# Kernel optimization log

Measured on AMD Instinct MI355X. Metric: run time of the kernel, lower is better.

The kernel has to match this reference:

```python
import jax, jax.numpy as jnp
import numpy as np

LAT, LONG = 16, 12
C_IN, C_MID = 128, 128
GROUPS = C_IN // 8          # conv groups and GroupNorm groups = 16
E = 200_000                 # number of projection entries (edges)
N = 4096                    # out_size (number of target messages)
PAD = LONG // 2
EPS = 1e-5


def setup_inputs() -> dict:
    key = jax.random.key(0)
    ks = jax.random.split(key, 8)
    x = jax.random.normal(ks[0], (E, C_IN), dtype=jnp.float32)
    proj_index = jax.random.randint(ks[1], (4, E), 0, N * LAT * LONG, dtype=jnp.int64 if jax.config.jax_enable_x64 else jnp.int32)
    proj_delta = jax.random.uniform(ks[2], (4, E), dtype=jnp.float32)
    proj_src_index = jax.random.randint(ks[3], (E,), 0, E, dtype=jnp.int64 if jax.config.jax_enable_x64 else jnp.int32)
    # grouped circular Conv1d: weight [out, in/groups, k] = [128, 2048/16, 12]
    fan_in = (C_IN * LAT // GROUPS) * LONG
    bound = 1.0 / np.sqrt(fan_in)
    conv_w = jax.random.uniform(ks[4], (C_MID, C_IN * LAT // GROUPS, LONG), dtype=jnp.float32, minval=-bound, maxval=bound)
    conv_b = jax.random.uniform(ks[5], (C_MID,), dtype=jnp.float32, minval=-bound, maxval=bound)
    gn_w = jnp.ones((C_MID,), dtype=jnp.float32)
    gn_b = jnp.zeros((C_MID,), dtype=jnp.float32)
    return {"x": x, "out_size": N, "proj_index": proj_index, "proj_delta": proj_delta,
            "proj_src_index": proj_src_index, "conv_w": conv_w, "conv_b": conv_b,
            "gn_w": gn_w, "gn_b": gn_b}


def reference(x, out_size, proj_index, proj_delta, proj_src_index, conv_w, conv_b, gn_w, gn_b):
    # ---- ProjectLatLongSphere: 4 weighted scatter-adds onto the sphere grid ----
    splat = x[proj_src_index]                              # [E, C]
    x_proj = jnp.zeros((out_size * LAT * LONG, C_IN), dtype=x.dtype)
    for i in range(4):                                      # fixed small unroll
        x_proj = x_proj.at[proj_index[i]].add(splat * proj_delta[i][:, None])
    # [N, lat*long, C] -> [N, C, lat*long] -> [N, C*lat, long]
    x_grid = x_proj.reshape(out_size, LAT * LONG, C_IN).transpose(0, 2, 1)
    x_grid = x_grid.reshape(out_size, C_IN * LAT, LONG)

    # ---- grouped circular Conv1d ----
    xp = jnp.concatenate([x_grid[..., -PAD:], x_grid, x_grid[..., :PAD]], axis=-1)  # [N, C*lat, long+2*pad]
    y = jax.lax.conv_general_dilated(
        xp, conv_w, window_strides=(1,), padding='VALID',
        dimension_numbers=('NCH', 'OIH', 'NCH'), feature_group_count=GROUPS)        # [N, C_MID, long+1]
    y = jax.nn.silu(y + conv_b[None, :, None])

    # ---- AvgPool1d(kernel=long) over first `long` positions ----
    y = jnp.mean(y[:, :, :LONG], axis=-1)                   # [N, C_MID]

    # ---- GroupNorm(num_groups=GROUPS) on [N, C_MID] ----
    g = y.reshape(out_size, GROUPS, C_MID // GROUPS)
    mu = jnp.mean(g, axis=-1, keepdims=True)
    var = jnp.var(g, axis=-1, keepdims=True)
    g = (g - mu) * jax.lax.rsqrt(var + EPS)
    return g.reshape(out_size, C_MID) * gn_w + gn_b
```

## Files before the change

kernel.cpp:

```cpp
#include <hip/hip_runtime.h>
#include <hip/hip_fp16.h>
#include <cstdint>

#define LATN 16
#define LONGN 12
#define PP 192
#define CIN 128
#define CMID 128
#define EPSV 1e-5f
#define SPLIT 4
#define CHB 32
#define TST 36
#define UMAXA 4

typedef float v2f __attribute__((ext_vector_type(2)));
typedef float f32x4 __attribute__((ext_vector_type(4)));
typedef _Float16 half8 __attribute__((ext_vector_type(8)));


__global__ void count2_kernel(const int* __restrict__ pidx, int* __restrict__ counts, int E) {
    int e = blockIdx.x * 256 + threadIdx.x;
    if (e >= E) return;
#pragma unroll
    for (int i = 0; i < 4; i++) {
        int v = pidx[i * E + e];
        atomicAdd(&counts[v], 1);
    }
}

__global__ void scan1_kernel(const int* __restrict__ cnt, int* __restrict__ startp,
                             int* __restrict__ bsum) {
    __shared__ int sd[1024];
    int t = threadIdx.x, b = blockIdx.x;
    int v = cnt[b * 1024 + t];
    sd[t] = v;
    __syncthreads();
    for (int off = 1; off < 1024; off <<= 1) {
        int x = (t >= off) ? sd[t - off] : 0;
        __syncthreads();
        sd[t] += x;
        __syncthreads();
    }
    startp[b * 1024 + t] = sd[t] - v;
    if (t == 1023) bsum[b] = sd[t];
}

__global__ void scan2_kernel(int* __restrict__ bsum, int* __restrict__ grand, int nb) {
    __shared__ int sd[1024];
    int t = threadIdx.x;
    int v = (t < nb) ? bsum[t] : 0;
    sd[t] = v;
    __syncthreads();
    for (int off = 1; off < 1024; off <<= 1) {
        int x = (t >= off) ? sd[t - off] : 0;
        __syncthreads();
        sd[t] += x;
        __syncthreads();
    }
    if (t < nb) bsum[t] = sd[t] - v;
    if (t == 1023) *grand = sd[1023];
}

__global__ void addback_kernel(int* __restrict__ startp, const int* __restrict__ bsum,
                               int* __restrict__ cur) {
    int v = blockIdx.x * 1024 + threadIdx.x;
    int s = startp[v] + bsum[blockIdx.x];
    startp[v] = s;
    cur[v] = s;
}

__global__ void record_kernel(const int* __restrict__ pidx, const int* __restrict__ src_idx,
                              const float* __restrict__ delta, int* __restrict__ cur,
                              uint2* __restrict__ rec, int E) {
    int e = blockIdx.x * 256 + threadIdx.x;
    if (e >= E) return;
    int src = src_idx[e];
#pragma unroll
    for (int i = 0; i < 4; i++) {
        int v = pidx[i * E + e];
        int p = v - (v / PP) * PP;
        int pos = atomicAdd(&cur[v], 1);
        rec[pos] = make_uint2((uint32_t)src | ((uint32_t)p << 18),
                              __float_as_uint(delta[i * E + e]));
    }
}

__global__ void wt2_kernel(const float* __restrict__ w, uint32_t* __restrict__ wt2) {
    int id = blockIdx.x * 256 + threadIdx.x;
    if (id >= CIN * 6 * CMID) return;
    int o = id & 127;
    int kp = (id >> 7) % 6;
    int i = id / (128 * 6);
    float a = w[(o * 128 + i) * 12 + 2 * kp];
    float b = w[(o * 128 + i) * 12 + 2 * kp + 1];
    __half2 h = __floats2half2_rn(a, b);
    wt2[id] = *reinterpret_cast<uint32_t*>(&h);
}


__global__ void wA_kernel(const float* __restrict__ w, _Float16* __restrict__ wA) {
    int id = blockIdx.x * 256 + threadIdx.x;
    if (id >= 16 * 6 * 48 * 64) return;
    int lane = id & 63;
    int rest = id >> 6;
    int s = rest % 48;
    int mt = (rest / 48) % 6;
    int g = rest / (48 * 6);
    int m = mt * 16 + (lane & 15);
    int o = m / 12;
    int t = m - o * 12;
    int og = g * 8 + o;
    _Float16 vals[8];
#pragma unroll
    for (int j = 0; j < 8; j++) {
        int kh = s * 32 + (lane >> 4) * 8 + j;
        int c = kh / PP;
        int p = kh - c * PP;
        int lat = p / LONGN;
        int ll = p - lat * LONGN;
        int k = (ll - t + 18) % 12;
        vals[j] = (_Float16)w[((og)*128 + c * 16 + lat) * 12 + k];
    }
    *(uint4*)(wA + (size_t)id * 8) = *(const uint4*)vals;
}


__global__ __launch_bounds__(256, 5) void scatter_kernel(
    const float* __restrict__ x, const uint2* __restrict__ rec,
    const int* __restrict__ start2, _Float16* __restrict__ grid) {
    __shared__ __align__(16) float tile[PP * TST];
    __shared__ int s2c[PP + 1];

    const int bid = blockIdx.x;
    const int n = bid >> 2;
    const int b = bid & 3;
    const int tid = threadIdx.x;

    {
        float4 zz = {0.f, 0.f, 0.f, 0.f};
        float4* t4 = (float4*)tile;
        for (int idx = tid; idx < PP * TST / 4; idx += 256) t4[idx] = zz;
        for (int idx = tid; idx < PP + 1; idx += 256) s2c[idx] = start2[n * PP + idx];
    }
    __syncthreads();

    {
        const int il = tid & 7;
        const int slot = tid >> 3;
        const int cbase = b * CHB + il * 4;
        const int e1 = s2c[slot * 6 + 6];
        for (int e = s2c[slot * 6]; e < e1; e += UMAXA) {
            uint2 rv[UMAXA];
            float4 xv[UMAXA];
#pragma unroll
            for (int u = 0; u < UMAXA; u++) {
                if (e + u < e1) rv[u] = rec[e + u];
            }
#pragma unroll
            for (int u = 0; u < UMAXA; u++) {
                if (e + u < e1) {
                    int src = (int)(rv[u].x & 0x3FFFFu);
                    xv[u] = *(const float4*)(x + (size_t)src * CIN + cbase);
                }
            }
#pragma unroll
            for (int u = 0; u < UMAXA; u++) {
                if (e + u < e1) {
                    float dl = __uint_as_float(rv[u].y);
                    int p = (int)(rv[u].x >> 18);
                    float* tp = tile + p * TST + (((il + (p & 7)) & 7) << 2);
                    float4 t = *(const float4*)tp;
                    t.x += xv[u].x * dl;
                    t.y += xv[u].y * dl;
                    t.z += xv[u].z * dl;
                    t.w += xv[u].w * dl;
                    *(float4*)tp = t;
                }
            }
        }
    }
    __syncthreads();

    {
        const int c = tid & 31;
        const int pc = tid >> 5;
        const int gch = b * CHB + c;
        _Float16* gdst = grid + ((size_t)n * CIN + gch) * PP;
        const int il = c >> 2;
        const int cm = c & 3;
#pragma unroll
        for (int j16 = 0; j16 < 3; j16++) {
            int pbase = pc * 24 + j16 * 8;
            _Float16 hh[8];
#pragma unroll
            for (int i = 0; i < 8; i++) {
                int p = pbase + i;
                hh[i] = (_Float16)tile[p * TST + ((((il + (p & 7)) & 7) << 2) + cm)];
            }
            *(uint4*)(gdst + pbase) = *(const uint4*)hh;
        }
    }
}


__global__ __launch_bounds__(128, 4) void gemm_kernel(
    const _Float16* __restrict__ grid, const _Float16* __restrict__ wA,
    const float* __restrict__ conv_b, const float* __restrict__ gn_w,
    const float* __restrict__ gn_b, float* __restrict__ out) {
    __shared__ float Clds[96 * 17];

    const int bid = blockIdx.x;
    const int g = bid >> 8;
    const int ntile = bid & 255;
    const int n_base = ntile * 16;
    const int tid = threadIdx.x;
    const int lane = tid & 63;
    const int wv = tid >> 6;

    const int nn = lane & 15;
    const int h = lane >> 4;

    const _Float16* bptr = grid + ((size_t)(n_base + nn) * CIN + g * 8) * PP + h * 8;
    const size_t abase = ((size_t)(g * 6 + wv * 3) * 48 * 64 + lane) * 8;
    const _Float16* a0 = wA + abase;
    const _Float16* a1 = wA + abase + (size_t)48 * 512;
    const _Float16* a2 = wA + abase + (size_t)96 * 512;

    f32x4 acc0 = {0.f, 0.f, 0.f, 0.f};
    f32x4 acc1 = {0.f, 0.f, 0.f, 0.f};
    f32x4 acc2 = {0.f, 0.f, 0.f, 0.f};

#pragma unroll 4
    for (int s = 0; s < 48; s++) {
        half8 bf = *(const half8*)(bptr + s * 32);
        half8 A0 = *(const half8*)(a0 + (size_t)s * 512);
        half8 A1 = *(const half8*)(a1 + (size_t)s * 512);
        half8 A2 = *(const half8*)(a2 + (size_t)s * 512);
        acc0 = __builtin_amdgcn_mfma_f32_16x16x32_f16(A0, bf, acc0, 0, 0, 0);
        acc1 = __builtin_amdgcn_mfma_f32_16x16x32_f16(A1, bf, acc1, 0, 0, 0);
        acc2 = __builtin_amdgcn_mfma_f32_16x16x32_f16(A2, bf, acc2, 0, 0, 0);
    }

    {
        int mbase = (wv * 3) * 16 + h * 4;
#pragma unroll
        for (int j = 0; j < 4; j++) Clds[(mbase + j) * 17 + nn] = acc0[j];
#pragma unroll
        for (int j = 0; j < 4; j++) Clds[(mbase + 16 + j) * 17 + nn] = acc1[j];
#pragma unroll
        for (int j = 0; j < 4; j++) Clds[(mbase + 32 + j) * 17 + nn] = acc2[j];
    }
    __syncthreads();

    {
        const int n8 = tid >> 3;
        const int o = tid & 7;
        const int oc = g * 8 + o;
        float bias = conv_b[oc];
        float sv = 0.f;
#pragma unroll
        for (int t = 0; t < 12; t++) {
            float z = Clds[(o * 12 + t) * 17 + n8] + bias;
            sv += z / (1.f + __expf(-z));
        }
        sv *= (1.f / 12.f);
        float s1 = sv, s2 = sv * sv;
#pragma unroll
        for (int m = 1; m < 8; m <<= 1) {
            s1 += __shfl_xor(s1, m);
            s2 += __shfl_xor(s2, m);
        }
        float mu = s1 * 0.125f;
        float var = fmaxf(s2 * 0.125f - mu * mu, 0.f);
        float inv = rsqrtf(var + EPSV);
        out[(size_t)(n_base + n8) * CMID + oc] = (sv - mu) * inv * gn_w[oc] + gn_b[oc];
    }
}


__global__ __launch_bounds__(256, 5) void fused_kernel(
    const float* __restrict__ x, const uint2* __restrict__ rec,
    const int* __restrict__ start2, const uint32_t* __restrict__ wt2,
    const float* __restrict__ conv_b, const float* __restrict__ gn_w,
    const float* __restrict__ gn_b, float* __restrict__ out) {
    __shared__ __align__(16) float tile[PP * TST];
    __shared__ int s2c[PP + 1];

    const int bid = blockIdx.x;
    const int n = bid >> 2;
    const int b = bid & 3;
    const int tid = threadIdx.x;

    {
        float4 zz = {0.f, 0.f, 0.f, 0.f};
        float4* t4 = (float4*)tile;
        for (int idx = tid; idx < PP * TST / 4; idx += 256) t4[idx] = zz;
        for (int idx = tid; idx < PP + 1; idx += 256) s2c[idx] = start2[n * PP + idx];
    }
    __syncthreads();

    {
        const int il = tid & 7;
        const int slot = tid >> 3;
        const int cbase = b * CHB + il * 4;
        const int e1 = s2c[slot * 6 + 6];
        float* tbase = tile + il * 4;
        for (int e = s2c[slot * 6]; e < e1; e += UMAXA) {
            uint2 rv[UMAXA];
            float4 xv[UMAXA];
#pragma unroll
            for (int u = 0; u < UMAXA; u++) {
                if (e + u < e1) rv[u] = rec[e + u];
            }
#pragma unroll
            for (int u = 0; u < UMAXA; u++) {
                if (e + u < e1) {
                    int src = (int)(rv[u].x & 0x3FFFFu);
                    xv[u] = *(const float4*)(x + (size_t)src * CIN + cbase);
                }
            }
#pragma unroll
            for (int u = 0; u < UMAXA; u++) {
                if (e + u < e1) {
                    float dl = __uint_as_float(rv[u].y);
                    int p = (int)(rv[u].x >> 18);
                    float* tp = tbase + p * TST;
                    float4 t = *(const float4*)tp;
                    t.x += xv[u].x * dl;
                    t.y += xv[u].y * dl;
                    t.z += xv[u].z * dl;
                    t.w += xv[u].w * dl;
                    *(float4*)tp = t;
                }
            }
        }
    }
    __syncthreads();

    const int o_local = tid & 31;
    const int q = tid >> 5;
    const int g_local = o_local >> 3;
    const int o = b * CHB + o_local;
    const int ch = g_local * 8 + q;

    v2f acc2[6];
#pragma unroll
    for (int u = 0; u < 6; u++) acc2[u] = (v2f)(0.f);

    const uint32_t* wcol = wt2 + (size_t)(q * LATN) * 6 * CMID + o;

#pragma unroll
    for (int lat = 0; lat < LATN; lat++) {
        float r[12];
#pragma unroll
        for (int j = 0; j < 12; j++)
            r[j] = tile[(lat * LONGN + j) * TST + ch];
        v2f rp[12];
#pragma unroll
        for (int j = 0; j < 12; j++) {
            rp[j].x = r[(j + 6) % 12];
            rp[j].y = r[(j + 7) % 12];
        }
        const uint32_t* wrow = wcol + (size_t)(lat * 6) * CMID;
#pragma unroll
        for (int kp = 0; kp < 6; kp++) {
            uint32_t wp = wrow[kp * CMID];
            __half2 h2 = *reinterpret_cast<__half2*>(&wp);
            float wlo = __half2float(h2.x);
            float whi = __half2float(h2.y);
            v2f wl2 = {wlo, wlo}, wh2 = {whi, whi};
#pragma unroll
            for (int u = 0; u < 6; u++) {
                acc2[u] += wl2 * rp[(2 * kp + 2 * u) % 12];
                acc2[u] += wh2 * rp[(2 * kp + 2 * u + 1) % 12];
            }
        }
    }
    __syncthreads();

    float* pbuf = tile;
#pragma unroll
    for (int u = 0; u < 6; u++) {
        pbuf[(q * 12 + 2 * u) * 32 + o_local] = acc2[u].x;
        pbuf[(q * 12 + 2 * u + 1) * 32 + o_local] = acc2[u].y;
    }
    __syncthreads();

    float* gbuf = tile + 8 * 12 * 32;
    float sv = 0.f;
    if (tid < 32) {
        float bias = conv_b[b * CHB + tid];
#pragma unroll
        for (int t = 0; t < 12; t++) {
            float z = bias;
#pragma unroll
            for (int qq = 0; qq < 8; qq++) z += pbuf[(qq * 12 + t) * 32 + tid];
            sv += z / (1.f + __expf(-z));
        }
        sv *= (1.f / 12.f);
        gbuf[tid] = sv;
    }
    __syncthreads();
    if (tid < 32) {
        int gb = tid & ~7;
        float mu = 0.f, m2 = 0.f;
#pragma unroll
        for (int j = 0; j < 8; j++) {
            float v = gbuf[gb + j];
            mu += v;
            m2 += v * v;
        }
        mu *= 0.125f;
        float var = m2 * 0.125f - mu * mu;
        var = fmaxf(var, 0.f);
        float inv = rsqrtf(var + EPSV);
        int oc = b * CHB + tid;
        out[(size_t)n * CMID + oc] = (sv - mu) * inv * gn_w[oc] + gn_b[oc];
    }
}

extern "C" void kernel_launch(void* const* d_in, const int* in_sizes, int n_in,
                              void* d_out, int out_size, void* d_ws, size_t ws_size,
                              hipStream_t stream) {
    const float* x = (const float*)d_in[0];
    const int* pidx = (const int*)d_in[2];
    const float* delta = (const float*)d_in[3];
    const int* src_idx = (const int*)d_in[4];
    const float* conv_w = (const float*)d_in[5];
    const float* conv_b = (const float*)d_in[6];
    const float* gn_w = (const float*)d_in[7];
    const float* gn_b = (const float*)d_in[8];
    float* out = (float*)d_out;

    int E = in_sizes[0] / CIN;
    int N = out_size / CMID;
    int ncells = N * PP;

    char* ws = (char*)d_ws;
    size_t off = 0;
    auto alloc = [&](size_t bytes) {
        size_t cur = off;
        off = (off + bytes + 255) & ~(size_t)255;
        return cur;
    };
    int* count2 = (int*)(ws + alloc((size_t)ncells * 4));
    int* start2 = (int*)(ws + alloc((size_t)(ncells + 1) * 4));
    int* bsum   = (int*)(ws + alloc((size_t)1024 * 4));
    uint2* rec  = (uint2*)(ws + alloc((size_t)4 * E * 8));
    uint32_t* wt2 = (uint32_t*)(ws + alloc((size_t)CIN * 6 * CMID * 4));
    size_t wA_off = alloc((size_t)16 * 6 * 48 * 64 * 8 * 2);
    size_t grid_off = alloc((size_t)N * CIN * PP * 2);
    _Float16* wA = (_Float16*)(ws + wA_off);
    _Float16* gridbuf = (_Float16*)(ws + grid_off);
    bool two_pass = (off <= ws_size);

    hipMemsetAsync(count2, 0, (size_t)ncells * 4, stream);

    int gE = (E + 255) / 256;
    int nb = ncells / 1024;
    count2_kernel<<<gE, 256, 0, stream>>>(pidx, count2, E);
    scan1_kernel<<<nb, 1024, 0, stream>>>(count2, start2, bsum);
    scan2_kernel<<<1, 1024, 0, stream>>>(bsum, start2 + ncells, nb);
    addback_kernel<<<nb, 1024, 0, stream>>>(start2, bsum, count2);
    record_kernel<<<gE, 256, 0, stream>>>(pidx, src_idx, delta, count2, rec, E);

    if (two_pass) {
        wA_kernel<<<(16 * 6 * 48 * 64 + 255) / 256, 256, 0, stream>>>(conv_w, wA);
        scatter_kernel<<<N * SPLIT, 256, 0, stream>>>(x, rec, start2, gridbuf);
        gemm_kernel<<<16 * 256, 128, 0, stream>>>(gridbuf, wA, conv_b, gn_w, gn_b, out);
    } else {
        wt2_kernel<<<(CIN * 6 * CMID + 255) / 256, 256, 0, stream>>>(conv_w, wt2);
        fused_kernel<<<N * SPLIT, 256, 0, stream>>>(x, rec, start2, wt2, conv_b, gn_w, gn_b, out);
    }
}
```

Baseline: 345.3 us.

## Enlarge gemm tile to 64 targets per block with register prefetch

The grouped-conv GEMM now gives each 256-thread block 64 targets instead of 16. Each wave computes a 48x32 sub-tile, so every A fragment is reused across two B fragments and weight loads are amortised. The loop software-prefetches the next step's A and B fragments into registers, and the block index is reordered so groups vary fastest. This adds register pressure and makes the grid smaller (1024 blocks instead of 4096), which may reduce occupancy and load balance.

```diff
diff --git a/kernel.cpp b/kernel.cpp
--- a/kernel.cpp
+++ b/kernel.cpp
@@ -203,77 +203,100 @@
 }
 
 
-__global__ __launch_bounds__(128, 4) void gemm_kernel(
+__global__ __launch_bounds__(256, 5) void gemm_kernel(
     const _Float16* __restrict__ grid, const _Float16* __restrict__ wA,
     const float* __restrict__ conv_b, const float* __restrict__ gn_w,
     const float* __restrict__ gn_b, float* __restrict__ out) {
-    __shared__ float Clds[96 * 17];
+    __shared__ float Clds[96 * 66];
 
     const int bid = blockIdx.x;
-    const int g = bid >> 8;
-    const int ntile = bid & 255;
-    const int n_base = ntile * 16;
+    const int g = bid & 15;
+    const int ntile = bid >> 4;
     const int tid = threadIdx.x;
     const int lane = tid & 63;
     const int wv = tid >> 6;
+    const int mh = wv & 1;
+    const int nh = wv >> 1;
 
     const int nn = lane & 15;
     const int h = lane >> 4;
 
-    const _Float16* bptr = grid + ((size_t)(n_base + nn) * CIN + g * 8) * PP + h * 8;
-    const size_t abase = ((size_t)(g * 6 + wv * 3) * 48 * 64 + lane) * 8;
-    const _Float16* a0 = wA + abase;
-    const _Float16* a1 = wA + abase + (size_t)48 * 512;
-    const _Float16* a2 = wA + abase + (size_t)96 * 512;
-
-    f32x4 acc0 = {0.f, 0.f, 0.f, 0.f};
-    f32x4 acc1 = {0.f, 0.f, 0.f, 0.f};
-    f32x4 acc2 = {0.f, 0.f, 0.f, 0.f};
+    const _Float16* a0 = wA + ((size_t)(g * 6 + mh * 3) * 48) * 512 + lane * 8;
+    const _Float16* a1 = a0 + (size_t)48 * 512;
+    const _Float16* a2 = a1 + (size_t)48 * 512;
+    const _Float16* b0 = grid + ((size_t)(ntile * 64 + nh * 32 + nn) * CIN + g * 8) * PP + h * 8;
+    const _Float16* b1 = b0 + (size_t)16 * CIN * PP;
+
+    f32x4 acc00 = {0.f, 0.f, 0.f, 0.f}, acc01 = {0.f, 0.f, 0.f, 0.f};
+    f32x4 acc10 = {0.f, 0.f, 0.f, 0.f}, acc11 = {0.f, 0.f, 0.f, 0.f};
+    f32x4 acc20 = {0.f, 0.f, 0.f, 0.f}, acc21 = {0.f, 0.f, 0.f, 0.f};
+
+    half8 cA0 = *(const half8*)(a0);
+    half8 cA1 = *(const half8*)(a1);
+    half8 cA2 = *(const half8*)(a2);
+    half8 cB0 = *(const half8*)(b0);
+    half8 cB1 = *(const half8*)(b1);
 
 #pragma unroll 4
     for (int s = 0; s < 48; s++) {
-        half8 bf = *(const half8*)(bptr + s * 32);
-        half8 A0 = *(const half8*)(a0 + (size_t)s * 512);
-        half8 A1 = *(const half8*)(a1 + (size_t)s * 512);
-        half8 A2 = *(const half8*)(a2 + (size_t)s * 512);
-        acc0 = __builtin_amdgcn_mfma_f32_16x16x32_f16(A0, bf, acc0, 0, 0, 0);
-        acc1 = __builtin_amdgcn_mfma_f32_16x16x32_f16(A1, bf, acc1, 0, 0, 0);
-        acc2 = __builtin_amdgcn_mfma_f32_16x16x32_f16(A2, bf, acc2, 0, 0, 0);
-    }
-
-    {
-        int mbase = (wv * 3) * 16 + h * 4;
-#pragma unroll
-        for (int j = 0; j < 4; j++) Clds[(mbase + j) * 17 + nn] = acc0[j];
-#pragma unroll
-        for (int j = 0; j < 4; j++) Clds[(mbase + 16 + j) * 17 + nn] = acc1[j];
-#pragma unroll
-        for (int j = 0; j < 4; j++) Clds[(mbase + 32 + j) * 17 + nn] = acc2[j];
-    }
-    __syncthreads();
-
-    {
-        const int n8 = tid >> 3;
+        half8 nA0 = cA0, nA1 = cA1, nA2 = cA2, nB0 = cB0, nB1 = cB1;
+        if (s + 1 < 48) {
+            nA0 = *(const half8*)(a0 + (size_t)(s + 1) * 512);
+            nA1 = *(const half8*)(a1 + (size_t)(s + 1) * 512);
+            nA2 = *(const half8*)(a2 + (size_t)(s + 1) * 512);
+            nB0 = *(const half8*)(b0 + (size_t)(s + 1) * 32);
+            nB1 = *(const half8*)(b1 + (size_t)(s + 1) * 32);
+        }
+        acc00 = __builtin_amdgcn_mfma_f32_16x16x32_f16(cA0, cB0, acc00, 0, 0, 0);
+        acc10 = __builtin_amdgcn_mfma_f32_16x16x32_f16(cA1, cB0, acc10, 0, 0, 0);
+        acc20 = __builtin_amdgcn_mfma_f32_16x16x32_f16(cA2, cB0, acc20, 0, 0, 0);
+        acc01 = __builtin_amdgcn_mfma_f32_16x16x32_f16(cA0, cB1, acc01, 0, 0, 0);
+        acc11 = __builtin_amdgcn_mfma_f32_16x16x32_f16(cA1, cB1, acc11, 0, 0, 0);
+        acc21 = __builtin_amdgcn_mfma_f32_16x16x32_f16(cA2, cB1, acc21, 0, 0, 0);
+        cA0 = nA0; cA1 = nA1; cA2 = nA2; cB0 = nB0; cB1 = nB1;
+    }
+
+    {
+        const int mbase = mh * 48 + h * 4;
+        const int ncol = nh * 32 + nn;
+#pragma unroll
+        for (int j = 0; j < 4; j++) {
+            Clds[(mbase + j) * 66 + ncol] = acc00[j];
+            Clds[(mbase + j) * 66 + ncol + 16] = acc01[j];
+            Clds[(mbase + 16 + j) * 66 + ncol] = acc10[j];
+            Clds[(mbase + 16 + j) * 66 + ncol + 16] = acc11[j];
+            Clds[(mbase + 32 + j) * 66 + ncol] = acc20[j];
+            Clds[(mbase + 32 + j) * 66 + ncol + 16] = acc21[j];
+        }
+    }
+    __syncthreads();
+
+    {
         const int o = tid & 7;
         const int oc = g * 8 + o;
-        float bias = conv_b[oc];
-        float sv = 0.f;
-#pragma unroll
-        for (int t = 0; t < 12; t++) {
-            float z = Clds[(o * 12 + t) * 17 + n8] + bias;
-            sv += z / (1.f + __expf(-z));
-        }
-        sv *= (1.f / 12.f);
-        float s1 = sv, s2 = sv * sv;
-#pragma unroll
-        for (int m = 1; m < 8; m <<= 1) {
-            s1 += __shfl_xor(s1, m);
-            s2 += __shfl_xor(s2, m);
-        }
-        float mu = s1 * 0.125f;
-        float var = fmaxf(s2 * 0.125f - mu * mu, 0.f);
-        float inv = rsqrtf(var + EPSV);
-        out[(size_t)(n_base + n8) * CMID + oc] = (sv - mu) * inv * gn_w[oc] + gn_b[oc];
+        const float bias = conv_b[oc];
+        const float gw = gn_w[oc], gb = gn_b[oc];
+#pragma unroll
+        for (int pp = 0; pp < 2; pp++) {
+            const int nl = (tid >> 3) + pp * 32;
+            float sv = 0.f;
+#pragma unroll
+            for (int t = 0; t < 12; t++) {
+                float z = Clds[(o * 12 + t) * 66 + nl] + bias;
+                sv += z / (1.f + __expf(-z));
+            }
+            sv *= (1.f / 12.f);
+            float s1 = sv, s2 = sv * sv;
+#pragma unroll
+            for (int m = 1; m < 8; m <<= 1) {
+                s1 += __shfl_xor(s1, m);
+                s2 += __shfl_xor(s2, m);
+            }
+            float mu = s1 * 0.125f;
+            float var = fmaxf(s2 * 0.125f - mu * mu, 0.f);
+            float inv = rsqrtf(var + EPSV);
+            out[(size_t)(ntile * 64 + nl) * CMID + oc] = (sv - mu) * inv * gw + gb;
+        }
     }
 }
 
@@ -467,7 +490,7 @@
     if (two_pass) {
         wA_kernel<<<(16 * 6 * 48 * 64 + 255) / 256, 256, 0, stream>>>(conv_w, wA);
         scatter_kernel<<<N * SPLIT, 256, 0, stream>>>(x, rec, start2, gridbuf);
-        gemm_kernel<<<16 * 256, 128, 0, stream>>>(gridbuf, wA, conv_b, gn_w, gn_b, out);
+        gemm_kernel<<<16 * 64, 256, 0, stream>>>(gridbuf, wA, conv_b, gn_w, gn_b, out);
     } else {
         wt2_kernel<<<(CIN * 6 * CMID + 255) / 256, 256, 0, stream>>>(conv_w, wt2);
         fused_kernel<<<N * SPLIT, 256, 0, stream>>>(x, rec, start2, wt2, conv_b, gn_w, gn_b, out);
```

Measured after the change: 320.4 us. 7.2% less time.
